# Performance work log

Measured on AMD Instinct MI355X. Metric: run time of the kernel, lower is better.

## Reference

```python
import jax, jax.numpy as jnp
import numpy as np

N_VOX = 200_000
C = 64
B, G = 2, 128  # batch size, grid resolution per axis
K = 27         # 3x3x3 kernel volume
EPS = 1e-5


def _build_coords_and_kernel_map(seed=0):
    """Build unique voxel coords on a [B,G,G,G] grid and the 27-offset kernel map.

    nbr[i, k] = row index of the voxel at coord[i] + offset[k], or N_VOX if absent
    (sentinel row that gathers zeros). This mirrors MinkowskiEngine's
    coordinate-hash in/out kernel maps for a stride-1 conv.
    """
    rng = np.random.default_rng(seed)
    total = B * G * G * G
    keys = np.sort(rng.choice(total, size=N_VOX, replace=False).astype(np.int64))
    z = keys % G
    y = (keys // G) % G
    x = (keys // (G * G)) % G
    b = keys // (G * G * G)
    offs = [(dx, dy, dz) for dx in (-1, 0, 1) for dy in (-1, 0, 1) for dz in (-1, 0, 1)]
    nbr = np.full((N_VOX, K), N_VOX, dtype=np.int64)
    for k, (dx, dy, dz) in enumerate(offs):
        nx, ny, nz = x + dx, y + dy, z + dz
        valid = (nx >= 0) & (nx < G) & (ny >= 0) & (ny < G) & (nz >= 0) & (nz < G)
        nkey = ((b * G + nx) * G + ny) * G + nz
        pos = np.clip(np.searchsorted(keys, nkey), 0, N_VOX - 1)
        found = valid & (keys[pos] == nkey)
        nbr[:, k] = np.where(found, pos, N_VOX)
    return jnp.asarray(nbr)


def setup_inputs() -> dict:
    key = jax.random.key(0)
    ks = jax.random.split(key, 12)
    w_scale = 1.0 / np.sqrt(K * C)
    inp = {
        "feats": jax.random.normal(ks[0], (N_VOX, C), jnp.float32),
        "nbr": _build_coords_and_kernel_map(),
        "W1": jax.random.normal(ks[1], (K, C, C), jnp.float32) * w_scale,
        "g1": 1.0 + 0.1 * jax.random.normal(ks[2], (C,), jnp.float32),
        "b1": 0.1 * jax.random.normal(ks[3], (C,), jnp.float32),
        "m1": 0.1 * jax.random.normal(ks[4], (C,), jnp.float32),
        "v1": jax.random.uniform(ks[5], (C,), jnp.float32, 0.5, 1.5),
        "W2": jax.random.normal(ks[6], (K, C, C), jnp.float32) * w_scale,
        "g2": 1.0 + 0.1 * jax.random.normal(ks[7], (C,), jnp.float32),
        "b2": 0.1 * jax.random.normal(ks[8], (C,), jnp.float32),
        "m2": 0.1 * jax.random.normal(ks[9], (C,), jnp.float32),
        "v2": jax.random.uniform(ks[10], (C,), jnp.float32, 0.5, 1.5),
    }
    return inp


def _bn(x, g, b, m, v):
    # MinkowskiBatchNorm, eval mode: per-channel affine with running stats
    return (x - m) * (g * jax.lax.rsqrt(v + EPS)) + b


def _sparse_conv(feats, nbr, W):
    # gather-GEMM-scatter sparse 3D conv over the precomputed kernel map.
    # Sentinel index N_VOX gathers the appended zero row (missing neighbor).
    fpad = jnp.concatenate([feats, jnp.zeros((1, feats.shape[1]), feats.dtype)], axis=0)
    out = jnp.zeros((feats.shape[0], W.shape[2]), feats.dtype)
    for k in range(W.shape[0]):  # fixed 27-tap loop (structural, not data dim)
        out = out + fpad[nbr[:, k]] @ W[k]
    return out


def reference(feats, nbr, W1, g1, b1, m1, v1, W2, g2, b2, m2, v2):
    h = jax.nn.relu(_bn(_sparse_conv(feats, nbr, W1), g1, b1, m1, v1))
    h = _bn(_sparse_conv(h, nbr, W2), g2, b2, m2, v2)
    # in_channels == out_channels and stride == 1 -> identity shortcut
    return jax.nn.relu(h + feats)
```

## Files before the change

kernel.cpp:

```cpp
#include <hip/hip_runtime.h>
#include <hip/hip_bf16.h>

#define NVOX 200000
#define NTAP 27
#define NSTR 68
#define OSTR 68
#define ROWB 128

typedef __bf16          bf16x8 __attribute__((ext_vector_type(8)));
typedef unsigned short  u16x8  __attribute__((ext_vector_type(8)));
typedef float           f32x4  __attribute__((ext_vector_type(4)));

#define FB_BYTES    ((size_t)(NVOX + 1) * ROWB)
#define WSHUF_BYTES (NTAP * 2 * 4 * 64 * 16)
#define FB_OFF      0
#define H_OFF       (FB_BYTES)
#define WS1_OFF     (2 * FB_BYTES)
#define WS2_OFF     (WS1_OFF + WSHUF_BYTES)
#define FLAG_OFF    (WS2_OFF + WSHUF_BYTES)

static __device__ __forceinline__ unsigned short f2bf_bits(float f) {
    __hip_bfloat16 h = __float2bfloat16(f);
    union { __hip_bfloat16 h; unsigned short u; } u; u.h = h; return u.u;
}
static __device__ __forceinline__ float bf2f(unsigned short s) {
    union { float f; unsigned u; } u; u.u = ((unsigned)s) << 16; return u.f;
}
static __device__ __forceinline__ float ld_param(const void* p, int c, int isbf) {
    return isbf ? bf2f(((const unsigned short*)p)[c]) : ((const float*)p)[c];
}
static __device__ __forceinline__ void gload_lds16(const void* gp, void* lp) {
    __builtin_amdgcn_global_load_lds(
        (const __attribute__((address_space(1))) void*)gp,
        (__attribute__((address_space(3))) void*)lp, 16, 0, 0);
}
static __device__ __forceinline__ int wave_isbf(const unsigned* v1w) {
    int l = threadIdx.x & 63;
    int ok = 1;
    if (l < 32) {
        unsigned w = v1w[l], lo = w & 0xFFFFu, hi = w >> 16;
        ok = (lo >= 0x3F00u && lo <= 0x3FC0u && hi >= 0x3F00u && hi <= 0x3FC0u);
    }
    return __all(ok);
}

__global__ __launch_bounds__(256)
void prep_kernel(const void* __restrict__ feats,
                 const void* __restrict__ W1, const void* __restrict__ W2,
                 const unsigned* __restrict__ v1w, const unsigned* __restrict__ nbrw,
                 uint4* __restrict__ fbuf, uint4* __restrict__ hbuf,
                 uint4* __restrict__ Ws1, uint4* __restrict__ Ws2,
                 int* __restrict__ flags) {
    const int bx = blockIdx.x;
    if (bx < 6250) {
        const int isbf = wave_isbf(v1w);
        size_t t = (size_t)bx * 256 + threadIdx.x;
        if (isbf) {
            fbuf[t] = ((const uint4*)feats)[t];
        } else {
            float4 a = ((const float4*)feats)[2 * t];
            float4 b = ((const float4*)feats)[2 * t + 1];
            union { uint4 q; unsigned short u[8]; } o;
            o.u[0] = f2bf_bits(a.x); o.u[1] = f2bf_bits(a.y);
            o.u[2] = f2bf_bits(a.z); o.u[3] = f2bf_bits(a.w);
            o.u[4] = f2bf_bits(b.x); o.u[5] = f2bf_bits(b.y);
            o.u[6] = f2bf_bits(b.z); o.u[7] = f2bf_bits(b.w);
            fbuf[t] = o.q;
        }
    } else if (bx < 6358) {
        const int isbf = wave_isbf(v1w);
        int t = (bx - 6250) * 256 + threadIdx.x;
        const void* W = (t < 13824) ? W1 : W2;
        uint4* Ws     = (t < 13824) ? Ws1 : Ws2;
        int f = (t < 13824) ? t : t - 13824;
        int k  = f / 512;
        int r  = f % 512;
        int kc = r / 256;
        int r2 = r % 256;
        int nc = r2 / 64;
        int l  = r2 % 64;
        int quad = l >> 4, li = l & 15;
        unsigned short tmp[8];
#pragma unroll
        for (int j = 0; j < 8; ++j) {
            int off = k * 4096 + (kc * 32 + quad * 8 + j) * 64 + (nc * 16 + li);
            tmp[j] = isbf ? ((const unsigned short*)W)[off]
                          : f2bf_bits(((const float*)W)[off]);
        }
        uint4 v;
        v.x = (unsigned)tmp[0] | ((unsigned)tmp[1] << 16);
        v.y = (unsigned)tmp[2] | ((unsigned)tmp[3] << 16);
        v.z = (unsigned)tmp[4] | ((unsigned)tmp[5] << 16);
        v.w = (unsigned)tmp[6] | ((unsigned)tmp[7] << 16);
        Ws[f] = v;
    } else {
        int t = threadIdx.x;
        if (t < 64) {
            int isbf = wave_isbf(v1w);
            int n64ok = 1;
#pragma unroll
            for (int i = 0; i < 8; ++i)
                if (nbrw[2 * (t * 8 + i) + 1] != 0u) n64ok = 0;
            int n64 = __all(n64ok);
            if (t == 0) { flags[0] = isbf; flags[1] = n64; }
        }
        uint4 z = make_uint4(0u, 0u, 0u, 0u);
        if (t >= 64 && t < 72) fbuf[(size_t)NVOX * 8 + (t - 64)] = z;
        if (t >= 72 && t < 80) hbuf[(size_t)NVOX * 8 + (t - 72)] = z;
    }
}

#define STAGE(kk, bp) do {                                                  \
    if ((mOR >> (kk)) & 1) {                                                \
        int ia_ = nbrLDS[(kk) * NSTR + r0];                                 \
        int ib_ = nbrLDS[(kk) * NSTR + r1];                                 \
        gload_lds16(srcB + (size_t)ia_ * ROWB + f0 * 16,                    \
                    (void*)((bp) + w * 128));                               \
        gload_lds16(srcB + (size_t)ib_ * ROWB + f1 * 16,                    \
                    (void*)((bp) + w * 128 + 64));                          \
    } } while (0)

#define LOADB(kk, B0, B1) do {                                              \
    B0 = Ws[(kk) * 512 + w * 64 + l];                                       \
    B1 = Ws[(kk) * 512 + 256 + w * 64 + l];                                 \
} while (0)

#define COMPUTE(kk, bp, B0, B1) do {                                        \
    _Pragma("unroll")                                                       \
    for (int g = 0; g < 4; ++g) {                                           \
        if ((mg[g] >> (kk)) & 1) {                                          \
            bf16x8 a0_ = *(const bf16x8*)((bp) + ro0[g]);                   \
            bf16x8 a1_ = *(const bf16x8*)((bp) + ro1[g]);                   \
            acc[g] = __builtin_amdgcn_mfma_f32_16x16x32_bf16(a0_, B0, acc[g], 0, 0, 0); \
            acc[g] = __builtin_amdgcn_mfma_f32_16x16x32_bf16(a1_, B1, acc[g], 0, 0, 0); \
        }                                                                   \
    }                                                                       \
} while (0)

__global__ __launch_bounds__(256, 6)
void conv_bn_kernel(const uint4* __restrict__ srcV,
                    const void* __restrict__ nbr,
                    const bf16x8* __restrict__ Ws,
                    const void* __restrict__ gg, const void* __restrict__ bb,
                    const void* __restrict__ mm, const void* __restrict__ vv,
                    const u16x8* __restrict__ resid,
                    const int* __restrict__ flags,
                    void* __restrict__ dst, int final_out) {
    __shared__ uint4 sm[1484];
    __shared__ int maskLDS[4];
    int*   nbrLDS = (int*)sm;
    uint4* at0    = sm + 459;
    uint4* at1    = at0 + 512;
    float* outLDS = (float*)sm;

    const int tid  = threadIdx.x;
    const int base = blockIdx.x * 64;
    const int isbf = flags[0];
    const int n64  = flags[1];
    const char* srcB = (const char*)srcV;

    if (tid < 4) maskLDS[tid] = 0;
    {
        for (int i = tid; i < NTAP * 64; i += 256) {
            int mvox = i / NTAP;
            int ktap = i - mvox * NTAP;
            long gi = (long)base * NTAP + i;
            int idx = n64 ? (int)((const long long*)nbr)[gi] : ((const int*)nbr)[gi];
            nbrLDS[ktap * NSTR + mvox] = idx;
        }
    }
    __syncthreads();

    if (tid < NTAP * 4) {
        int k = tid >> 2, g = tid & 3;
        const int4* p = (const int4*)&nbrLDS[k * NSTR + g * 16];
        int4 a = p[0], b = p[1], c = p[2], d = p[3];
        int mn = min(min(min(a.x, a.y), min(a.z, a.w)),
                     min(min(min(b.x, b.y), min(b.z, b.w)),
                         min(min(min(c.x, c.y), min(c.z, c.w)),
                             min(min(d.x, d.y), min(d.z, d.w)))));
        if (mn < NVOX) atomicOr(&maskLDS[g], 1 << k);
    }
    __syncthreads();

    const int w = tid >> 6, l = tid & 63;
    const int quad = l >> 4, li = l & 15;

    int mg[4];
#pragma unroll
    for (int g = 0; g < 4; ++g) mg[g] = __builtin_amdgcn_readfirstlane(maskLDS[g]);
    const int mOR = mg[0] | mg[1] | mg[2] | mg[3];

    const int s0 = w * 128 + l;
    const int s1 = s0 + 64;
    const int r0 = s0 >> 3, f0 = (s0 - r0) & 7;
    const int r1 = s1 >> 3, f1 = (s1 - r1) & 7;
    int ro0[4], ro1[4];
#pragma unroll
    for (int g = 0; g < 4; ++g) {
        int row = g * 16 + li;
        ro0[g] = row * 8 + ((quad + row) & 7);
        ro1[g] = row * 8 + ((quad + 4 + row) & 7);
    }

    f32x4 acc[4];
#pragma unroll
    for (int g = 0; g < 4; ++g) acc[g] = (f32x4){0.f, 0.f, 0.f, 0.f};

    bf16x8 xB0, xB1, yB0, yB1;

    STAGE(0, at0);
    LOADB(0, xB0, xB1);
    __syncthreads();

    for (int k = 0; k < 26; k += 2) {
        STAGE(k + 1, at1);
        LOADB(k + 1, yB0, yB1);
        COMPUTE(k, at0, xB0, xB1);
        __syncthreads();
        STAGE(k + 2, at0);
        LOADB(k + 2, xB0, xB1);
        COMPUTE(k + 1, at1, yB0, yB1);
        __syncthreads();
    }
    COMPUTE(26, at0, xB0, xB1);

    const int c = w * 16 + li;
    float scale = ld_param(gg, c, isbf) * rsqrtf(ld_param(vv, c, isbf) + 1e-5f);
    float offs  = ld_param(bb, c, isbf) - ld_param(mm, c, isbf) * scale;

    __syncthreads();
#pragma unroll
    for (int g = 0; g < 4; ++g)
#pragma unroll
        for (int r = 0; r < 4; ++r)
            outLDS[(g * 16 + quad * 4 + r) * OSTR + c] = acc[g][r] * scale + offs;
    __syncthreads();

    {
        int trow = tid >> 2, cc = tid & 3;
        long grow = base + trow;
        const float4* lp = (const float4*)&outLDS[trow * OSTR + cc * 16];
        float4 q0 = lp[0], q1 = lp[1], q2 = lp[2], q3 = lp[3];
        float vals[16] = {q0.x, q0.y, q0.z, q0.w, q1.x, q1.y, q1.z, q1.w,
                          q2.x, q2.y, q2.z, q2.w, q3.x, q3.y, q3.z, q3.w};

        if (resid) {
            const u16x8* rp = resid + grow * 8 + cc * 2;
            u16x8 r0v = rp[0], r1v = rp[1];
#pragma unroll
            for (int j = 0; j < 8; ++j) { vals[j] += bf2f(r0v[j]); vals[8 + j] += bf2f(r1v[j]); }
        }
#pragma unroll
        for (int j = 0; j < 16; ++j) vals[j] = fmaxf(vals[j], 0.f);

        const int store_bf = (!final_out) || isbf;
        if (store_bf) {
            u16x8 o0, o1;
#pragma unroll
            for (int j = 0; j < 8; ++j) { o0[j] = f2bf_bits(vals[j]); o1[j] = f2bf_bits(vals[8 + j]); }
            u16x8* dp = (u16x8*)dst + grow * 8 + cc * 2;
            dp[0] = o0; dp[1] = o1;
        } else {
            float4* dp = (float4*)dst + grow * 16 + cc * 4;
            dp[0] = (float4){vals[0], vals[1], vals[2], vals[3]};
            dp[1] = (float4){vals[4], vals[5], vals[6], vals[7]};
            dp[2] = (float4){vals[8], vals[9], vals[10], vals[11]};
            dp[3] = (float4){vals[12], vals[13], vals[14], vals[15]};
        }
    }
}

extern "C" void kernel_launch(void* const* d_in, const int* in_sizes, int n_in,
                              void* d_out, int out_size, void* d_ws, size_t ws_size,
                              hipStream_t stream) {
    const void* feats = d_in[0];
    const void* nbr   = d_in[1];
    const void* W1    = d_in[2];
    const void* g1    = d_in[3];
    const void* b1    = d_in[4];
    const void* m1    = d_in[5];
    const void* v1    = d_in[6];
    const void* W2    = d_in[7];
    const void* g2    = d_in[8];
    const void* b2    = d_in[9];
    const void* m2    = d_in[10];
    const void* v2    = d_in[11];

    char* ws = (char*)d_ws;
    uint4* fbuf = (uint4*)(ws + FB_OFF);
    uint4* hbuf = (uint4*)(ws + H_OFF);
    uint4* Ws1  = (uint4*)(ws + WS1_OFF);
    uint4* Ws2  = (uint4*)(ws + WS2_OFF);
    int*   flags = (int*)(ws + FLAG_OFF);

    prep_kernel<<<dim3(6359), dim3(256), 0, stream>>>(
        feats, W1, W2, (const unsigned*)v1, (const unsigned*)nbr,
        fbuf, hbuf, Ws1, Ws2, flags);

    conv_bn_kernel<<<dim3(NVOX / 64), dim3(256), 0, stream>>>(
        fbuf, nbr, (const bf16x8*)Ws1, g1, b1, m1, v1,
        nullptr, flags, hbuf, 0);

    conv_bn_kernel<<<dim3(NVOX / 64), dim3(256), 0, stream>>>(
        hbuf, nbr, (const bf16x8*)Ws2, g2, b2, m2, v2,
        (const u16x8*)fbuf, flags, d_out, 1);
}
```

Measured before the change: 259.5 us.

## Stage two taps per LDS buffer to halve barriers in the gather-MFMA loop

Each LDS buffer now holds two taps of gathered neighbour rows instead of one, so each barrier covers four taps rather than two and the tap loop runs seven iterations. Tap indices past 26 are skipped through the mask bits, and weight loads are clamped to tap 26. Each wave now decides whether to stage a tap from its own 16-row group's neighbour mask rather than the OR across all groups, which skips more gathers for empty neighbours. The price is double the LDS for the tile, so the launch bound drops from 6 to 4 blocks per CU and fewer blocks are resident to hide gather latency.

```diff
diff --git a/kernel.cpp b/kernel.cpp
--- a/kernel.cpp
+++ b/kernel.cpp
@@ -17,7 +17,7 @@
 #define H_OFF       (FB_BYTES)
 #define WS1_OFF     (2 * FB_BYTES)
 #define WS2_OFF     (WS1_OFF + WSHUF_BYTES)
-#define FLAG_OFF    (WS2_OFF + WSHUF_BYTES)
+#define FLAG_OFF    (WS2_OFF + WSHUF_BYTES + 32768)
 
 static __device__ __forceinline__ unsigned short f2bf_bits(float f) {
     __hip_bfloat16 h = __float2bfloat16(f);
@@ -110,19 +110,20 @@
     }
 }
 
-#define STAGE(kk, bp) do {                                                  \
-    if ((mOR >> (kk)) & 1) {                                                \
+#define STG(kk, bp, off) do {                                               \
+    if ((mgw >> (kk)) & 1) {                                                \
         int ia_ = nbrLDS[(kk) * NSTR + r0];                                 \
         int ib_ = nbrLDS[(kk) * NSTR + r1];                                 \
         gload_lds16(srcB + (size_t)ia_ * ROWB + f0 * 16,                    \
-                    (void*)((bp) + w * 128));                               \
+                    (void*)((bp) + (off) + w * 128));                       \
         gload_lds16(srcB + (size_t)ib_ * ROWB + f1 * 16,                    \
-                    (void*)((bp) + w * 128 + 64));                          \
+                    (void*)((bp) + (off) + w * 128 + 64));                  \
     } } while (0)
 
 #define LOADB(kk, B0, B1) do {                                              \
-    B0 = Ws[(kk) * 512 + w * 64 + l];                                       \
-    B1 = Ws[(kk) * 512 + 256 + w * 64 + l];                                 \
+    int kc_ = (kk) < 26 ? (kk) : 26;                                        \
+    B0 = Ws[kc_ * 512 + w * 64 + l];                                        \
+    B1 = Ws[kc_ * 512 + 256 + w * 64 + l];                                  \
 } while (0)
 
 #define COMPUTE(kk, bp, B0, B1) do {                                        \
@@ -137,7 +138,7 @@
     }                                                                       \
 } while (0)
 
-__global__ __launch_bounds__(256, 6)
+__global__ __launch_bounds__(256, 4)
 void conv_bn_kernel(const uint4* __restrict__ srcV,
                     const void* __restrict__ nbr,
                     const bf16x8* __restrict__ Ws,
@@ -146,11 +147,11 @@
                     const u16x8* __restrict__ resid,
                     const int* __restrict__ flags,
                     void* __restrict__ dst, int final_out) {
-    __shared__ uint4 sm[1484];
+    __shared__ uint4 sm[459 + 2048];
     __shared__ int maskLDS[4];
     int*   nbrLDS = (int*)sm;
     uint4* at0    = sm + 459;
-    uint4* at1    = at0 + 512;
+    uint4* at1    = at0 + 1024;
     float* outLDS = (float*)sm;
 
     const int tid  = threadIdx.x;
@@ -189,7 +190,7 @@
     int mg[4];
 #pragma unroll
     for (int g = 0; g < 4; ++g) mg[g] = __builtin_amdgcn_readfirstlane(maskLDS[g]);
-    const int mOR = mg[0] | mg[1] | mg[2] | mg[3];
+    const int mgw = __builtin_amdgcn_readfirstlane(maskLDS[w]);
 
     const int s0 = w * 128 + l;
     const int s1 = s0 + 64;
@@ -209,27 +210,32 @@
 
     bf16x8 xB0, xB1, yB0, yB1;
 
-    STAGE(0, at0);
+    STG(0, at0, 0);
+    STG(1, at0, 512);
     LOADB(0, xB0, xB1);
     __syncthreads();
 
-    for (int k = 0; k < 26; k += 2) {
-        STAGE(k + 1, at1);
+    for (int k = 0; k < 28; k += 4) {
+        STG(k + 2, at1, 0);
+        STG(k + 3, at1, 512);
         LOADB(k + 1, yB0, yB1);
         COMPUTE(k, at0, xB0, xB1);
+        LOADB(k + 2, xB0, xB1);
+        COMPUTE(k + 1, at0 + 512, yB0, yB1);
         __syncthreads();
-        STAGE(k + 2, at0);
-        LOADB(k + 2, xB0, xB1);
-        COMPUTE(k + 1, at1, yB0, yB1);
+        STG(k + 4, at0, 0);
+        STG(k + 5, at0, 512);
+        LOADB(k + 3, yB0, yB1);
+        COMPUTE(k + 2, at1, xB0, xB1);
+        LOADB(k + 4, xB0, xB1);
+        COMPUTE(k + 3, at1 + 512, yB0, yB1);
         __syncthreads();
     }
-    COMPUTE(26, at0, xB0, xB1);
 
     const int c = w * 16 + li;
     float scale = ld_param(gg, c, isbf) * rsqrtf(ld_param(vv, c, isbf) + 1e-5f);
     float offs  = ld_param(bb, c, isbf) - ld_param(mm, c, isbf) * scale;
 
-    __syncthreads();
 #pragma unroll
     for (int g = 0; g < 4; ++g)
 #pragma unroll
```

New measurement: 291.8 us. +12.4%, slower.

## Load neighbor map contiguously into LDS and gate gather per wave group

Applied to the files above, without the earlier changes.

Stores the per-block neighbor indices in their natural voxel-major layout so the global load is a straight contiguous copy with no per-element divide and transpose. The per-tap staging of gathered rows is now gated on the mask of the 16-row group that this wave stages, rather than the OR over all four groups, which skips more gathers for empty taps. Launch bounds are raised to 7 blocks per CU to allow more occupancy. The mask reduction now reads strided LDS entries and may see bank conflicts, and the tighter register budget could cause spills.

```diff
diff --git a/kernel.cpp b/kernel.cpp
--- a/kernel.cpp
+++ b/kernel.cpp
@@ -3,7 +3,6 @@
 
 #define NVOX 200000
 #define NTAP 27
-#define NSTR 68
 #define OSTR 68
 #define ROWB 128
 
@@ -110,14 +109,14 @@
     }
 }
 
-#define STAGE(kk, bp) do {                                                  \
-    if ((mOR >> (kk)) & 1) {                                                \
-        int ia_ = nbrLDS[(kk) * NSTR + r0];                                 \
-        int ib_ = nbrLDS[(kk) * NSTR + r1];                                 \
+#define STG(kk, bp) do {                                                    \
+    if ((mgw >> (kk)) & 1) {                                                \
+        int ia_ = nbrLDS[r0 * NTAP + (kk)];                                 \
+        int ib_ = nbrLDS[r1 * NTAP + (kk)];                                 \
         gload_lds16(srcB + (size_t)ia_ * ROWB + f0 * 16,                    \
                     (void*)((bp) + w * 128));                               \
         gload_lds16(srcB + (size_t)ib_ * ROWB + f1 * 16,                    \
-                    (void*)((bp) + w * 128 + 64));                          \
+                    (void*)((bp) + w * 128 + 64));                         \
     } } while (0)
 
 #define LOADB(kk, B0, B1) do {                                              \
@@ -137,7 +136,7 @@
     }                                                                       \
 } while (0)
 
-__global__ __launch_bounds__(256, 6)
+__global__ __launch_bounds__(256, 7)
 void conv_bn_kernel(const uint4* __restrict__ srcV,
                     const void* __restrict__ nbr,
                     const bf16x8* __restrict__ Ws,
@@ -146,12 +145,12 @@
                     const u16x8* __restrict__ resid,
                     const int* __restrict__ flags,
                     void* __restrict__ dst, int final_out) {
-    __shared__ uint4 sm[1484];
-    __shared__ int maskLDS[4];
-    int*   nbrLDS = (int*)sm;
-    uint4* at0    = sm + 459;
+    __shared__ __align__(16) int smi[5828];
+    int*   nbrLDS = smi;
+    uint4* at0    = (uint4*)(smi + 1728);
     uint4* at1    = at0 + 512;
-    float* outLDS = (float*)sm;
+    int*   maskLDS = smi + 5824;
+    float* outLDS = (float*)smi;
 
     const int tid  = threadIdx.x;
     const int base = blockIdx.x * 64;
@@ -160,25 +159,23 @@
     const char* srcB = (const char*)srcV;
 
     if (tid < 4) maskLDS[tid] = 0;
+    __syncthreads();
     {
-        for (int i = tid; i < NTAP * 64; i += 256) {
-            int mvox = i / NTAP;
-            int ktap = i - mvox * NTAP;
-            long gi = (long)base * NTAP + i;
-            int idx = n64 ? (int)((const long long*)nbr)[gi] : ((const int*)nbr)[gi];
-            nbrLDS[ktap * NSTR + mvox] = idx;
+        if (!n64) {
+            const int* np = (const int*)nbr + (long)base * NTAP;
+            for (int i = tid; i < 64 * NTAP; i += 256) nbrLDS[i] = np[i];
+        } else {
+            const long long* np = (const long long*)nbr + (long)base * NTAP;
+            for (int i = tid; i < 64 * NTAP; i += 256) nbrLDS[i] = (int)np[i];
         }
     }
     __syncthreads();
 
     if (tid < NTAP * 4) {
         int k = tid >> 2, g = tid & 3;
-        const int4* p = (const int4*)&nbrLDS[k * NSTR + g * 16];
-        int4 a = p[0], b = p[1], c = p[2], d = p[3];
-        int mn = min(min(min(a.x, a.y), min(a.z, a.w)),
-                     min(min(min(b.x, b.y), min(b.z, b.w)),
-                         min(min(min(c.x, c.y), min(c.z, c.w)),
-                             min(min(d.x, d.y), min(d.z, d.w)))));
+        int mn = 0x7fffffff;
+#pragma unroll
+        for (int r = 0; r < 16; ++r) mn = min(mn, nbrLDS[(g * 16 + r) * NTAP + k]);
         if (mn < NVOX) atomicOr(&maskLDS[g], 1 << k);
     }
     __syncthreads();
@@ -189,7 +186,7 @@
     int mg[4];
 #pragma unroll
     for (int g = 0; g < 4; ++g) mg[g] = __builtin_amdgcn_readfirstlane(maskLDS[g]);
-    const int mOR = mg[0] | mg[1] | mg[2] | mg[3];
+    const int mgw = __builtin_amdgcn_readfirstlane(maskLDS[w]);
 
     const int s0 = w * 128 + l;
     const int s1 = s0 + 64;
@@ -209,16 +206,16 @@
 
     bf16x8 xB0, xB1, yB0, yB1;
 
-    STAGE(0, at0);
+    STG(0, at0);
     LOADB(0, xB0, xB1);
     __syncthreads();
 
     for (int k = 0; k < 26; k += 2) {
-        STAGE(k + 1, at1);
+        STG(k + 1, at1);
         LOADB(k + 1, yB0, yB1);
         COMPUTE(k, at0, xB0, xB1);
         __syncthreads();
-        STAGE(k + 2, at0);
+        STG(k + 2, at0);
         LOADB(k + 2, xB0, xB1);
         COMPUTE(k + 1, at1, yB0, yB1);
         __syncthreads();
```

New measurement: 241.6 us. -6.9%, faster.
